# Performance work log

Measured on AMD Instinct MI355X. Metric: run time of the kernel, lower is better.

The kernel has to match this reference:

```python
import jax, jax.numpy as jnp
import numpy as np

IN_FEATURES = 1024
OUT_FEATURES = 1024
NUM_EXPERTS = 4
RANK = 16  # total_rank=64 / num_experts=4, rem=0 -> equal ranks
NETWORK_ALPHA = 64.0


def setup_inputs() -> dict:
    key = jax.random.key(0)
    k1, k2, k3, k4 = jax.random.split(key, 4)
    hidden_states = jax.random.normal(k1, (4, 4096, IN_FEATURES), dtype=jnp.float32)
    alpha = jax.random.uniform(k2, (4, NUM_EXPERTS), dtype=jnp.float32)
    # down: K Linear(in, r) weights, each [r, in], init std=1/r (as in torch init)
    down_w = jax.random.normal(k3, (NUM_EXPERTS, RANK, IN_FEATURES), dtype=jnp.float32) / RANK
    # up: K Linear(r, out) weights, each [out, r]. Torch inits these to zero,
    # which would make the output identically zero; use small random values so
    # the reference exercises the full math.
    up_w = jax.random.normal(k4, (NUM_EXPERTS, OUT_FEATURES, RANK), dtype=jnp.float32) * 0.02
    return {"hidden_states": hidden_states, "alpha": alpha, "down_w": down_w, "up_w": up_w}


def reference(hidden_states, alpha, down_w, up_w):
    # hidden_states: [B, N, D]; alpha: [B, K]
    # down_w: [K, r, D]; up_w: [K, out, r]
    scale = NETWORK_ALPHA / RANK  # network_alpha / rank_per_expert (equal ranks)
    # per-expert down projection: [B, K, N, r]
    low = jnp.einsum('bnd,krd->bknr', hidden_states, down_w)
    # up projection + scale + alpha-weighted sum over experts, fused: [B, N, out]
    out = jnp.einsum('bknr,kor,bk->bno', low, up_w, alpha) * scale
    return out
```

## Files before the change

### kernel.cpp

```cpp
#include <hip/hip_runtime.h>

namespace {

typedef short  bf16x8 __attribute__((ext_vector_type(8)));
typedef float  f32x4  __attribute__((ext_vector_type(4)));

constexpr int D = 1024;
constexpr int O = 1024;

__device__ __forceinline__ short f2bf(float f) {
    unsigned u = __builtin_bit_cast(unsigned, f);
    u += 0x7fffu + ((u >> 16) & 1u);
    return (short)(u >> 16);
}

__device__ __forceinline__ bf16x8 cvt8(const float4 a, const float4 b) {
    bf16x8 v;
    v[0] = f2bf(a.x); v[1] = f2bf(a.y); v[2] = f2bf(a.z); v[3] = f2bf(a.w);
    v[4] = f2bf(b.x); v[5] = f2bf(b.y); v[6] = f2bf(b.z); v[7] = f2bf(b.w);
    return v;
}

__device__ __forceinline__ float4 ld4(const float* p) {
    return *reinterpret_cast<const float4*>(p);
}

struct StageRegs { float4 a[4]; float4 b[4]; };

__device__ __forceinline__ void issue_dw(const float* __restrict__ dw, int c, int t,
                                         StageRegs& r) {
#pragma unroll
    for (int i = 0; i < 4; ++i) {
        const int e = i * 512 + t, kr = e >> 5, cc = e & 31;
        const float* sp = dw + (size_t)kr * D + c * 256 + cc * 8;
        r.a[i] = ld4(sp);
        r.b[i] = ld4(sp + 4);
    }
}
__device__ __forceinline__ void write_p1(short* buf, int t, const StageRegs& r) {
#pragma unroll
    for (int i = 0; i < 4; ++i) {
        const int e = i * 512 + t, kr = e >> 5, cc = e & 31;
        *reinterpret_cast<bf16x8*>(&buf[kr * 264 + cc * 8]) = cvt8(r.a[i], r.b[i]);
    }
}

__global__ void __launch_bounds__(512) lora_mfma_k(
        const float* __restrict__ hs,
        const float* __restrict__ alpha,
        const float* __restrict__ dw,
        const float* __restrict__ uw,
        float* __restrict__ out) {
    __shared__ __align__(16) short bs[2][64 * 264];
    __shared__ __align__(16) short lowb[4][16][72];
    __shared__ float pacc[4][16][64];

    const int t    = threadIdx.x;
    const int w    = t >> 6;
    const int lane = t & 63;
    const int fr   = lane & 15;
    const int kgi  = lane >> 4;
    const int kg   = kgi * 8;
    const int rt   = w >> 1;
    const int kh   = w & 1;
    const int rowblk = blockIdx.x * 64;
    const int b      = rowblk >> 12;
    const int myrow  = rowblk + rt * 16 + fr;
    const float* apb = hs + (size_t)myrow * D + kh * 128 + kg;

    StageRegs rg;
    issue_dw(dw, 0, t, rg);

    float4 pf[8];
#pragma unroll
    for (int ks = 0; ks < 4; ++ks) {
        pf[2 * ks]     = ld4(apb + ks * 32);
        pf[2 * ks + 1] = ld4(apb + ks * 32 + 4);
    }

    bf16x8 wreg[16];
#pragma unroll
    for (int nt2l = 0; nt2l < 8; ++nt2l)
#pragma unroll
        for (int h = 0; h < 2; ++h) {
            const int kr0 = h * 32 + kg;
            const int k   = kr0 >> 4;
            const int r0  = kr0 & 15;
            const float* sp = uw + (size_t)k * 16384
                                 + (size_t)(w * 128 + nt2l * 16 + fr) * 16 + r0;
            wreg[nt2l * 2 + h] = cvt8(ld4(sp), ld4(sp + 4));
        }

    write_p1(&bs[0][0], t, rg);
    __syncthreads();

    f32x4 acc[4];
#pragma unroll
    for (int nt = 0; nt < 4; ++nt) acc[nt] = (f32x4){0.f, 0.f, 0.f, 0.f};

#pragma unroll
    for (int c = 0; c < 4; ++c) {
        bf16x8 av[4];
#pragma unroll
        for (int ks = 0; ks < 4; ++ks) av[ks] = cvt8(pf[2 * ks], pf[2 * ks + 1]);

        if (c < 3) {
            const float* ap = apb + (c + 1) * 256;
#pragma unroll
            for (int ks = 0; ks < 4; ++ks) {
                pf[2 * ks]     = ld4(ap + ks * 32);
                pf[2 * ks + 1] = ld4(ap + ks * 32 + 4);
            }
            issue_dw(dw, c + 1, t, rg);
        }

#pragma unroll
        for (int ks = 0; ks < 4; ++ks)
#pragma unroll
            for (int nt = 0; nt < 4; ++nt) {
                const bf16x8 bv = *reinterpret_cast<const bf16x8*>(
                    &bs[c & 1][(nt * 16 + fr) * 264 + kh * 128 + ks * 32 + kg]);
                acc[nt] = __builtin_amdgcn_mfma_f32_16x16x32_bf16(av[ks], bv, acc[nt], 0, 0, 0);
            }

        if (c < 3) {
            write_p1(&bs[(c + 1) & 1][0], t, rg);
            __syncthreads();
        }
    }

    if (kh) {
#pragma unroll
        for (int nt = 0; nt < 4; ++nt)
#pragma unroll
            for (int j = 0; j < 4; ++j)
                pacc[rt][nt * 4 + j][lane] = acc[nt][j];
    }
    __syncthreads();
    if (!kh) {
#pragma unroll
        for (int nt = 0; nt < 4; ++nt) {
            const float sc = alpha[b * 4 + nt] * 4.0f;
#pragma unroll
            for (int j = 0; j < 4; ++j) {
                const float v = (acc[nt][j] + pacc[rt][nt * 4 + j][lane]) * sc;
                lowb[rt][kgi * 4 + j][nt * 16 + fr] = f2bf(v);
            }
        }
    }
    __syncthreads();

#pragma unroll
    for (int rt2 = 0; rt2 < 4; ++rt2) {
        const bf16x8 pa0 = *reinterpret_cast<const bf16x8*>(&lowb[rt2][fr][kg]);
        const bf16x8 pa1 = *reinterpret_cast<const bf16x8*>(&lowb[rt2][fr][32 + kg]);
        float* op = out + (size_t)(rowblk + rt2 * 16 + kgi * 4) * O + w * 128;
#pragma unroll
        for (int nt2l = 0; nt2l < 8; ++nt2l) {
            f32x4 c2 = (f32x4){0.f, 0.f, 0.f, 0.f};
            c2 = __builtin_amdgcn_mfma_f32_16x16x32_bf16(pa0, wreg[nt2l * 2],     c2, 0, 0, 0);
            c2 = __builtin_amdgcn_mfma_f32_16x16x32_bf16(pa1, wreg[nt2l * 2 + 1], c2, 0, 0, 0);
#pragma unroll
            for (int j = 0; j < 4; ++j)
                op[(size_t)j * O + nt2l * 16 + fr] = c2[j];
        }
    }
}

}

extern "C" void kernel_launch(void* const* d_in, const int* in_sizes, int n_in,
                              void* d_out, int out_size, void* d_ws, size_t ws_size,
                              hipStream_t stream) {
    const float* hs    = (const float*)d_in[0];
    const float* alpha = (const float*)d_in[1];
    const float* dw    = (const float*)d_in[2];
    const float* uw    = (const float*)d_in[3];
    float* outp = (float*)d_out;

    hipLaunchKernelGGL(lora_mfma_k, dim3(256), dim3(512), 0, stream,
                       hs, alpha, dw, uw, outp);
}
```

Measured before the change: 32.74 us.

## Split fused LoRA kernel into down-projection and up-projection kernels

```diff
diff --git a/kernel.cpp b/kernel.cpp
--- a/kernel.cpp
+++ b/kernel.cpp
@@ -45,14 +45,12 @@
     }
 }
 
-__global__ void __launch_bounds__(512) lora_mfma_k(
+__global__ void __launch_bounds__(512) lora_low_k(
         const float* __restrict__ hs,
         const float* __restrict__ alpha,
         const float* __restrict__ dw,
-        const float* __restrict__ uw,
-        float* __restrict__ out) {
+        short* __restrict__ lowg) {
     __shared__ __align__(16) short bs[2][64 * 264];
-    __shared__ __align__(16) short lowb[4][16][72];
     __shared__ float pacc[4][16][64];
 
     const int t    = threadIdx.x;
@@ -77,19 +75,6 @@
         pf[2 * ks]     = ld4(apb + ks * 32);
         pf[2 * ks + 1] = ld4(apb + ks * 32 + 4);
     }
-
-    bf16x8 wreg[16];
-#pragma unroll
-    for (int nt2l = 0; nt2l < 8; ++nt2l)
-#pragma unroll
-        for (int h = 0; h < 2; ++h) {
-            const int kr0 = h * 32 + kg;
-            const int k   = kr0 >> 4;
-            const int r0  = kr0 & 15;
-            const float* sp = uw + (size_t)k * 16384
-                                 + (size_t)(w * 128 + nt2l * 16 + fr) * 16 + r0;
-            wreg[nt2l * 2 + h] = cvt8(ld4(sp), ld4(sp + 4));
-        }
 
     write_p1(&bs[0][0], t, rg);
     __syncthreads();
@@ -144,26 +129,47 @@
 #pragma unroll
             for (int j = 0; j < 4; ++j) {
                 const float v = (acc[nt][j] + pacc[rt][nt * 4 + j][lane]) * sc;
-                lowb[rt][kgi * 4 + j][nt * 16 + fr] = f2bf(v);
+                lowg[(size_t)(rowblk + rt * 16 + kgi * 4 + j) * 64 + nt * 16 + fr] = f2bf(v);
             }
         }
     }
-    __syncthreads();
+}
 
+__global__ void __launch_bounds__(256) lora_up_k(
+        const short* __restrict__ lowg,
+        const float* __restrict__ uw,
+        float* __restrict__ out) {
+    const int t    = threadIdx.x;
+    const int w    = t >> 6;
+    const int lane = t & 63;
+    const int fr   = lane & 15;
+    const int kgi  = lane >> 4;
+    const int kg   = kgi * 8;
+    const int row0 = blockIdx.x * 16;
+
+    bf16x8 wreg[32];
 #pragma unroll
-    for (int rt2 = 0; rt2 < 4; ++rt2) {
-        const bf16x8 pa0 = *reinterpret_cast<const bf16x8*>(&lowb[rt2][fr][kg]);
-        const bf16x8 pa1 = *reinterpret_cast<const bf16x8*>(&lowb[rt2][fr][32 + kg]);
-        float* op = out + (size_t)(rowblk + rt2 * 16 + kgi * 4) * O + w * 128;
+    for (int n2 = 0; n2 < 16; ++n2)
 #pragma unroll
-        for (int nt2l = 0; nt2l < 8; ++nt2l) {
-            f32x4 c2 = (f32x4){0.f, 0.f, 0.f, 0.f};
-            c2 = __builtin_amdgcn_mfma_f32_16x16x32_bf16(pa0, wreg[nt2l * 2],     c2, 0, 0, 0);
-            c2 = __builtin_amdgcn_mfma_f32_16x16x32_bf16(pa1, wreg[nt2l * 2 + 1], c2, 0, 0, 0);
+        for (int h = 0; h < 2; ++h) {
+            const int kr0 = h * 32 + kg;
+            const float* sp = uw + (size_t)(kr0 >> 4) * 16384
+                                 + (size_t)(w * 256 + n2 * 16 + fr) * 16 + (kr0 & 15);
+            wreg[n2 * 2 + h] = cvt8(ld4(sp), ld4(sp + 4));
+        }
+
+    const short* lp = lowg + (size_t)(row0 + fr) * 64;
+    const bf16x8 pa0 = *reinterpret_cast<const bf16x8*>(lp + kg);
+    const bf16x8 pa1 = *reinterpret_cast<const bf16x8*>(lp + 32 + kg);
+
+    float* op = out + (size_t)(row0 + fr) * O + w * 256;
 #pragma unroll
-            for (int j = 0; j < 4; ++j)
-                op[(size_t)j * O + nt2l * 16 + fr] = c2[j];
-        }
+    for (int n2 = 0; n2 < 16; ++n2) {
+        f32x4 c2 = (f32x4){0.f, 0.f, 0.f, 0.f};
+        c2 = __builtin_amdgcn_mfma_f32_16x16x32_bf16(wreg[n2 * 2],     pa0, c2, 0, 0, 0);
+        c2 = __builtin_amdgcn_mfma_f32_16x16x32_bf16(wreg[n2 * 2 + 1], pa1, c2, 0, 0, 0);
+        const float4 vs = make_float4(c2[0], c2[1], c2[2], c2[3]);
+        *reinterpret_cast<float4*>(op + n2 * 16 + kgi * 4) = vs;
     }
 }
 
@@ -176,8 +182,9 @@
     const float* alpha = (const float*)d_in[1];
     const float* dw    = (const float*)d_in[2];
     const float* uw    = (const float*)d_in[3];
+    short* lowg = (short*)d_ws;
     float* outp = (float*)d_out;
 
-    hipLaunchKernelGGL(lora_mfma_k, dim3(256), dim3(512), 0, stream,
-                       hs, alpha, dw, uw, outp);
+    hipLaunchKernelGGL(lora_low_k, dim3(256),  dim3(512), 0, stream, hs, alpha, dw, lowg);
+    hipLaunchKernelGGL(lora_up_k,  dim3(1024), dim3(256), 0, stream, lowg, uw, outp);
 }
```

Measured after the change: 50.15 us. +53.2%, slower.
